# Optimization experiments

Hardware: AMD Instinct MI355X
Metric: run time of the kernel (lower is better)

Reference implementation:

```python
import jax, jax.numpy as jnp
import numpy as np
from jax.scipy.special import logsumexp

NODES = 128
K = 8
N = 4096  # num data samples; must equal M (original code stacks (N,) with (M,))
Z = NODES * (NODES - 1) // 2


def setup_inputs() -> dict:
    key = jax.random.key(0)
    k1, k2, k3 = jax.random.split(key, 3)
    X = jax.random.normal(k1, (N, NODES), dtype=jnp.float32)
    noise = jax.random.normal(k2, (N, NODES), dtype=jnp.float32)
    theta = jax.random.normal(k3, (K, 2, Z), dtype=jnp.float32)
    logc = jnp.zeros((K,), dtype=jnp.float32)
    return {"X": X, "noise": noise, "theta": theta, "logc": logc}


def reference(X, noise, theta, logc):
    n = X.shape[0]
    m = noise.shape[0]
    nodes = X.shape[1]
    iu, ju = np.triu_indices(nodes, k=1)  # static pair indices, z = nodes*(nodes-1)//2

    def mixture_logprob(A):
        # A: (S, nodes) -> per-component log prob summed over all node pairs, then
        # logsumexp over the K mixture components with weights logc.
        d = A[:, iu] - A[:, ju]                      # (S, z) pairwise phase diffs
        lp = (jnp.einsum('kz,sz->ks', theta[:, 0], jnp.cos(d))
              + jnp.einsum('kz,sz->ks', theta[:, 1], jnp.sin(d)))  # (K, S)
        return logsumexp(lp + logc[:, None], axis=0)  # (S,)

    lp_data = mixture_logprob(X)      # (n,)
    lp_noise = mixture_logprob(noise)  # (m,) == (n,)

    logN = jnp.log(jnp.float32(n))
    logM = jnp.log(jnp.float32(m))
    # log_nx = log_ny = 0 in the original code
    log_J1_denom = jnp.logaddexp(logN + lp_data, logM)
    log_J2_denom = jnp.logaddexp(logN + lp_noise, logM)
    J = (jnp.mean(logN + lp_data - log_J1_denom)
         + jnp.mean(logN - log_J2_denom))
    return J
```

## Files before the change

### kernel.cpp

```cpp
#include <hip/hip_runtime.h>
#include <hip/hip_bf16.h>
#include <math.h>

#define NODES 128
#define KMIX  8
#define NSAMP 4096
#define STOT  8192
#define ZPAIR 8128
#define FDIM  256

using bf16x8 = __attribute__((ext_vector_type(8))) short;
using f32x4  = __attribute__((ext_vector_type(4))) float;

#define OF_F   ((size_t)0)
#define OF_M   (OF_F + (size_t)STOT * FDIM / 2)
#define OF_LP4 (OF_M + (size_t)KMIX * FDIM * FDIM / 2)
#define OF_PT  (OF_LP4 + (size_t)4 * KMIX * STOT)
#define OF_CT  (OF_PT + 32)

__device__ __forceinline__ float bf2f(short u) {
    union { unsigned u32; float f; } cv;
    cv.u32 = ((unsigned)(unsigned short)u) << 16;
    return cv.f;
}
__device__ __forceinline__ short f2bf(float f) {
    union { float f; unsigned u32; } cv; cv.f = f;
    unsigned r = cv.u32 + 0x7fff + ((cv.u32 >> 16) & 1);
    return (short)(r >> 16);
}
__device__ __forceinline__ float softplusf(float x) {
    return fmaxf(x, 0.0f) + log1pf(expf(-fabsf(x)));
}

#define FEAT_BLOCKS (STOT * NODES / 256)
#define WB_BLOCKS   (KMIX * FDIM * FDIM / 256)

__global__ void prep_kernel(const float* __restrict__ X, const float* __restrict__ noise,
                            const float* __restrict__ theta,
                            short* __restrict__ F, short* __restrict__ W,
                            unsigned* __restrict__ ctr) {
    const int b = blockIdx.x, t = threadIdx.x;
    if (b == 0 && t == 0) *ctr = 0u;
    if (b < FEAT_BLOCKS) {
        int idx = b * 256 + t;
        int s = idx >> 7, i = idx & 127;
        float v = (s < NSAMP) ? X[idx] : noise[idx - NSAMP * NODES];
        float sv, cv;
        __sincosf(v, &sv, &cv);
        F[(size_t)s * FDIM + i]       = f2bf(cv);
        F[(size_t)s * FDIM + 128 + i] = f2bf(sv);
    } else {
        int idx = (b - FEAT_BLOCKS) * 256 + t;
        int j = idx & 255, i = (idx >> 8) & 255, k = idx >> 16;
        int a = i & 127, bb = j & 127;
        int hi = i >> 7, hj = j >> 7;
        float val = 0.0f;
        if (a != bb) {
            int p = a < bb ? a : bb;
            int q = a < bb ? bb : a;
            int z = p * 127 - (p * (p - 1)) / 2 + (q - p - 1);
            if (hi == hj) {
                val = 0.5f * theta[(size_t)(k * 2 + 0) * ZPAIR + z];
            } else if (hi == 1 && hj == 0) {
                float t1 = theta[(size_t)(k * 2 + 1) * ZPAIR + z];
                val = (a < bb) ? t1 : -t1;
            }
        }
        W[idx] = f2bf(val);
    }
}

__global__ __launch_bounds__(256, 2) void gemm_fused(
        const short* __restrict__ F, const short* __restrict__ M,
        float* __restrict__ lp2) {
    __shared__ short Ft[2][128 * 64];
    __shared__ short Mt[2][128 * 64];

    const int bid = blockIdx.x;
    const int k   = bid >> 6;
    const int st  = bid & 63;
    const int sbase = st * 128;

    const int t = threadIdx.x;
    const int wid = t >> 6, lane = t & 63;
    const int wm = wid >> 1, wn = wid & 1;

    const short* Mk = M + (size_t)k * FDIM * FDIM;

    const int rg = lane >> 3;
    const int sc = (lane & 7) ^ rg;

    f32x4 acc0[4][4] = {};
    f32x4 acc1[4][4] = {};

    auto stageF = [&](int buf, int c) {
        #pragma unroll
        for (int q = 0; q < 4; q++) {
            int g = wid * 4 + q;
            const short* src = F + ((size_t)(sbase + g * 8 + rg)) * FDIM + c * 64 + sc * 8;
            __builtin_amdgcn_global_load_lds((const unsigned*)src,
                                             (unsigned*)&Ft[buf][g * 512], 16, 0, 0);
        }
    };
    auto stageW = [&](int buf, int ihrow, int c) {
        #pragma unroll
        for (int q = 0; q < 4; q++) {
            int g = wid * 4 + q;
            const short* src = Mk + ((size_t)(ihrow * 128 + g * 8 + rg)) * FDIM + c * 64 + sc * 8;
            __builtin_amdgcn_global_load_lds((const unsigned*)src,
                                             (unsigned*)&Mt[buf][g * 512], 16, 0, 0);
        }
    };

    const int rlow = lane & 15, kq = lane >> 4;

    auto compute = [&](int fbuf, int mbuf, f32x4 (&acc)[4][4]) {
        bf16x8 afr[4][2], bfr[4][2];
        #pragma unroll
        for (int m = 0; m < 4; m++) {
            int row = wm * 64 + m * 16 + rlow;
            #pragma unroll
            for (int kk = 0; kk < 2; kk++) {
                int c16 = (kk * 4 + kq) ^ (row & 7);
                afr[m][kk] = *(const bf16x8*)&Ft[fbuf][row * 64 + c16 * 8];
            }
        }
        #pragma unroll
        for (int n = 0; n < 4; n++) {
            int row = wn * 64 + n * 16 + rlow;
            #pragma unroll
            for (int kk = 0; kk < 2; kk++) {
                int c16 = (kk * 4 + kq) ^ (row & 7);
                bfr[n][kk] = *(const bf16x8*)&Mt[mbuf][row * 64 + c16 * 8];
            }
        }
        #pragma unroll
        for (int m = 0; m < 4; m++)
            #pragma unroll
            for (int n = 0; n < 4; n++)
                #pragma unroll
                for (int kk = 0; kk < 2; kk++)
                    acc[m][n] = __builtin_amdgcn_mfma_f32_16x16x32_bf16(
                        afr[m][kk], bfr[n][kk], acc[m][n], 0, 0, 0);
    };

    stageF(0, 0); stageW(0, 0, 0);
    stageW(1, 1, 0);
    __syncthreads();
    compute(0, 0, acc0);
    __syncthreads();
    stageF(1, 1); stageW(0, 0, 1);
    __syncthreads();
    compute(0, 1, acc1);
    __syncthreads();
    stageW(1, 1, 1);
    __syncthreads();
    compute(1, 0, acc0);
    __syncthreads();
    stageF(0, 2); stageW(0, 1, 2);
    __syncthreads();
    compute(1, 1, acc1);
    __syncthreads();
    stageF(1, 3); stageW(1, 1, 3);
    __syncthreads();
    compute(0, 0, acc1);
    __syncthreads();
    compute(1, 1, acc1);

    float psum[4][4];
    #pragma unroll
    for (int m = 0; m < 4; m++) {
        #pragma unroll
        for (int q = 0; q < 4; q++) {
            int srow = wm * 64 + m * 16 + kq * 4 + q;
            const short* fr0 = F + (size_t)(sbase + srow) * FDIM + wn * 64 + rlow;
            float p = 0.0f;
            #pragma unroll
            for (int n = 0; n < 4; n++)
                p += bf2f(fr0[n * 16]) * acc0[m][n][q];
            #pragma unroll
            for (int n = 0; n < 4; n++)
                p += bf2f(fr0[128 + n * 16]) * acc1[m][n][q];
            psum[m][q] = p;
        }
    }
    #pragma unroll
    for (int off = 1; off < 16; off <<= 1)
        #pragma unroll
        for (int m = 0; m < 4; m++)
            #pragma unroll
            for (int q = 0; q < 4; q++)
                psum[m][q] += __shfl_xor(psum[m][q], off, 64);

    if (rlow == 0) {
        #pragma unroll
        for (int m = 0; m < 4; m++)
            #pragma unroll
            for (int q = 0; q < 4; q++) {
                int srow = wm * 64 + m * 16 + kq * 4 + q;
                lp2[((size_t)wn * KMIX + k) * STOT + sbase + srow] = psum[m][q];
            }
    }
}

__global__ void reduce_kernel(const float* __restrict__ lp2,
                              const float* __restrict__ logc,
                              float* __restrict__ partials,
                              unsigned* __restrict__ counter,
                              float* __restrict__ out) {
    const int t = threadIdx.x;
    const int s = blockIdx.x * 256 + t;

    float v[KMIX];
    #pragma unroll
    for (int k = 0; k < KMIX; k++) {
        v[k] = lp2[((size_t)0 * KMIX + k) * STOT + s]
             + lp2[((size_t)1 * KMIX + k) * STOT + s]
             + logc[k];
    }
    float mx = v[0];
    #pragma unroll
    for (int k = 1; k < KMIX; k++) mx = fmaxf(mx, v[k]);
    float sum = 0.0f;
    #pragma unroll
    for (int k = 0; k < KMIX; k++) sum += expf(v[k] - mx);
    const float lp = mx + logf(sum);

    const float term = (s < NSAMP) ? -softplusf(-lp) : -softplusf(lp);

    float bsum = term;
    #pragma unroll
    for (int off = 32; off; off >>= 1) bsum += __shfl_down(bsum, off);
    __shared__ float wsum[4];
    if ((t & 63) == 0) wsum[t >> 6] = bsum;
    __syncthreads();

    if (t == 0) {
        partials[blockIdx.x] = wsum[0] + wsum[1] + wsum[2] + wsum[3];
        __threadfence();
        unsigned old = atomicAdd(counter, 1u);
        if (old == 31u) {
            __threadfence();
            float tot = 0.0f;
            #pragma unroll
            for (int b = 0; b < 32; b++) tot += partials[b];
            out[0] = tot * (1.0f / (float)NSAMP);
        }
    }
}

extern "C" void kernel_launch(void* const* d_in, const int* in_sizes, int n_in,
                              void* d_out, int out_size, void* d_ws, size_t ws_size,
                              hipStream_t stream) {
    (void)in_sizes; (void)n_in; (void)out_size; (void)ws_size;
    const float* X     = (const float*)d_in[0];
    const float* noise = (const float*)d_in[1];
    const float* theta = (const float*)d_in[2];
    const float* logc  = (const float*)d_in[3];
    float* out = (float*)d_out;
    float* ws  = (float*)d_ws;

    short*    Fb    = (short*)(ws + OF_F);
    short*    Wb    = (short*)(ws + OF_M);
    float*    lp2   = ws + OF_LP4;
    float*    parts = ws + OF_PT;
    unsigned* ctr   = (unsigned*)(ws + OF_CT);

    prep_kernel<<<FEAT_BLOCKS + WB_BLOCKS, 256, 0, stream>>>(X, noise, theta, Fb, Wb, ctr);
    gemm_fused<<<KMIX * (STOT / 128), 256, 0, stream>>>(Fb, Wb, lp2);
    reduce_kernel<<<STOT / 256, 256, 0, stream>>>(lp2, logc, parts, ctr, out);
}
```

Measured before the change: 26.71 us.

## Overlap global-to-LDS staging with MFMA using explicit waitcnt and barriers

Splits the compute step into LDS fragment loads and MFMA issue. It replaces __syncthreads with hand-placed s_waitcnt vmcnt/lgkmcnt plus s_barrier, so the next tile's global_load_lds staging is issued before the current tile's MFMAs and overlaps them. This removes full drains of outstanding memory ops at each barrier. The risk is that the vmcnt counts are hand-tuned, and a miscount could read LDS data that is stale or not yet loaded.

```diff
diff --git a/kernel.cpp b/kernel.cpp
--- a/kernel.cpp
+++ b/kernel.cpp
@@ -17,6 +17,10 @@
 #define OF_LP4 (OF_M + (size_t)KMIX * FDIM * FDIM / 2)
 #define OF_PT  (OF_LP4 + (size_t)4 * KMIX * STOT)
 #define OF_CT  (OF_PT + 32)
+
+#define VMC(N) asm volatile("s_waitcnt vmcnt(" #N ")" ::: "memory")
+#define LGKM0  asm volatile("s_waitcnt lgkmcnt(0)" ::: "memory")
+#define SBAR   asm volatile("s_barrier" ::: "memory")
 
 __device__ __forceinline__ float bf2f(short u) {
     union { unsigned u32; float f; } cv;
@@ -114,8 +118,8 @@
 
     const int rlow = lane & 15, kq = lane >> 4;
 
-    auto compute = [&](int fbuf, int mbuf, f32x4 (&acc)[4][4]) {
-        bf16x8 afr[4][2], bfr[4][2];
+    bf16x8 afr[4][2], bfr[4][2];
+    auto loadA = [&](int fbuf) {
         #pragma unroll
         for (int m = 0; m < 4; m++) {
             int row = wm * 64 + m * 16 + rlow;
@@ -125,6 +129,8 @@
                 afr[m][kk] = *(const bf16x8*)&Ft[fbuf][row * 64 + c16 * 8];
             }
         }
+    };
+    auto loadB = [&](int mbuf) {
         #pragma unroll
         for (int n = 0; n < 4; n++) {
             int row = wn * 64 + n * 16 + rlow;
@@ -134,6 +140,8 @@
                 bfr[n][kk] = *(const bf16x8*)&Mt[mbuf][row * 64 + c16 * 8];
             }
         }
+    };
+    auto mfma = [&](f32x4 (&acc)[4][4]) {
         #pragma unroll
         for (int m = 0; m < 4; m++)
             #pragma unroll
@@ -144,28 +152,34 @@
                         afr[m][kk], bfr[n][kk], acc[m][n], 0, 0, 0);
     };
 
-    stageF(0, 0); stageW(0, 0, 0);
-    stageW(1, 1, 0);
-    __syncthreads();
-    compute(0, 0, acc0);
-    __syncthreads();
+    stageF(0, 0); stageW(0, 0, 0); stageW(1, 1, 0);
+
+    VMC(4); SBAR;
+    loadA(0); loadB(0);
+    LGKM0; SBAR;
     stageF(1, 1); stageW(0, 0, 1);
-    __syncthreads();
-    compute(0, 1, acc1);
-    __syncthreads();
+    mfma(acc0);
+    VMC(8); SBAR;
+    loadA(0); loadB(1);
+    LGKM0; SBAR;
     stageW(1, 1, 1);
-    __syncthreads();
-    compute(1, 0, acc0);
-    __syncthreads();
+    mfma(acc1);
+    VMC(4); SBAR;
+    loadA(1); loadB(0);
+    LGKM0; SBAR;
     stageF(0, 2); stageW(0, 1, 2);
-    __syncthreads();
-    compute(1, 1, acc1);
-    __syncthreads();
+    mfma(acc0);
+    VMC(8); SBAR;
+    loadA(1); loadB(1);
+    LGKM0; SBAR;
     stageF(1, 3); stageW(1, 1, 3);
-    __syncthreads();
-    compute(0, 0, acc1);
-    __syncthreads();
-    compute(1, 1, acc1);
+    mfma(acc1);
+    VMC(8); SBAR;
+    loadA(0); loadB(0);
+    mfma(acc1);
+    VMC(0); SBAR;
+    loadA(1); loadB(1);
+    mfma(acc1);
 
     float psum[4][4];
     #pragma unroll
```

Measured after the change: 26.53 us. Within noise of the previous version (-0.7%).

## Split GEMM across 8 waves, vectorize prep, and make lp layout sample-major

Applied to the files above, without the earlier changes.

The GEMM block grows from 4 to 8 waves, each owning a 64x32 output tile instead of 64x64. This halves per-wave accumulators and staging work, aiming at more latency hiding and occupancy, and MFMA runs get raised priority via s_setprio. The feature prep now processes four values per thread with vector loads and stores. Partial log-probs are stored sample-major with four column partials per component, so the reduce kernel reads contiguous float4s. The cost is more partial sums to combine and more shuffle work per wave.

```diff
diff --git a/kernel.cpp b/kernel.cpp
--- a/kernel.cpp
+++ b/kernel.cpp
@@ -14,8 +14,8 @@
 
 #define OF_F   ((size_t)0)
 #define OF_M   (OF_F + (size_t)STOT * FDIM / 2)
-#define OF_LP4 (OF_M + (size_t)KMIX * FDIM * FDIM / 2)
-#define OF_PT  (OF_LP4 + (size_t)4 * KMIX * STOT)
+#define OF_LP  (OF_M + (size_t)KMIX * FDIM * FDIM / 2)
+#define OF_PT  (OF_LP + (size_t)32 * STOT)
 #define OF_CT  (OF_PT + 32)
 
 __device__ __forceinline__ float bf2f(short u) {
@@ -32,8 +32,8 @@
     return fmaxf(x, 0.0f) + log1pf(expf(-fabsf(x)));
 }
 
-#define FEAT_BLOCKS (STOT * NODES / 256)
-#define WB_BLOCKS   (KMIX * FDIM * FDIM / 256)
+#define FEAT_BLOCKS4 (STOT * NODES / 4 / 256)
+#define WB_BLOCKS    (KMIX * FDIM * FDIM / 256)
 
 __global__ void prep_kernel(const float* __restrict__ X, const float* __restrict__ noise,
                             const float* __restrict__ theta,
@@ -41,16 +41,22 @@
                             unsigned* __restrict__ ctr) {
     const int b = blockIdx.x, t = threadIdx.x;
     if (b == 0 && t == 0) *ctr = 0u;
-    if (b < FEAT_BLOCKS) {
-        int idx = b * 256 + t;
-        int s = idx >> 7, i = idx & 127;
-        float v = (s < NSAMP) ? X[idx] : noise[idx - NSAMP * NODES];
-        float sv, cv;
-        __sincosf(v, &sv, &cv);
-        F[(size_t)s * FDIM + i]       = f2bf(cv);
-        F[(size_t)s * FDIM + 128 + i] = f2bf(sv);
+    if (b < FEAT_BLOCKS4) {
+        int idx4 = (b * 256 + t) * 4;
+        int s = idx4 >> 7, i = idx4 & 127;
+        const float* src = (s < NSAMP) ? (X + idx4) : (noise + (idx4 - NSAMP * NODES));
+        f32x4 v = *(const f32x4*)src;
+        short cb[4], sb[4];
+        #pragma unroll
+        for (int q = 0; q < 4; q++) {
+            float sv, cv;
+            __sincosf(v[q], &sv, &cv);
+            cb[q] = f2bf(cv); sb[q] = f2bf(sv);
+        }
+        *(short4*)&F[(size_t)s * FDIM + i]       = *(short4*)cb;
+        *(short4*)&F[(size_t)s * FDIM + 128 + i] = *(short4*)sb;
     } else {
-        int idx = (b - FEAT_BLOCKS) * 256 + t;
+        int idx = (b - FEAT_BLOCKS4) * 256 + t;
         int j = idx & 255, i = (idx >> 8) & 255, k = idx >> 16;
         int a = i & 127, bb = j & 127;
         int hi = i >> 7, hj = j >> 7;
@@ -70,9 +76,9 @@
     }
 }
 
-__global__ __launch_bounds__(256, 2) void gemm_fused(
+__global__ __launch_bounds__(512, 4) void gemm_fused(
         const short* __restrict__ F, const short* __restrict__ M,
-        float* __restrict__ lp2) {
+        float* __restrict__ lp32) {
     __shared__ short Ft[2][128 * 64];
     __shared__ short Mt[2][128 * 64];
 
@@ -83,20 +89,20 @@
 
     const int t = threadIdx.x;
     const int wid = t >> 6, lane = t & 63;
-    const int wm = wid >> 1, wn = wid & 1;
+    const int wm = wid >> 2, wn = wid & 3;
 
     const short* Mk = M + (size_t)k * FDIM * FDIM;
 
     const int rg = lane >> 3;
     const int sc = (lane & 7) ^ rg;
 
-    f32x4 acc0[4][4] = {};
-    f32x4 acc1[4][4] = {};
+    f32x4 acc0[4][2] = {};
+    f32x4 acc1[4][2] = {};
 
     auto stageF = [&](int buf, int c) {
         #pragma unroll
-        for (int q = 0; q < 4; q++) {
-            int g = wid * 4 + q;
+        for (int q = 0; q < 2; q++) {
+            int g = wid * 2 + q;
             const short* src = F + ((size_t)(sbase + g * 8 + rg)) * FDIM + c * 64 + sc * 8;
             __builtin_amdgcn_global_load_lds((const unsigned*)src,
                                              (unsigned*)&Ft[buf][g * 512], 16, 0, 0);
@@ -104,8 +110,8 @@
     };
     auto stageW = [&](int buf, int ihrow, int c) {
         #pragma unroll
-        for (int q = 0; q < 4; q++) {
-            int g = wid * 4 + q;
+        for (int q = 0; q < 2; q++) {
+            int g = wid * 2 + q;
             const short* src = Mk + ((size_t)(ihrow * 128 + g * 8 + rg)) * FDIM + c * 64 + sc * 8;
             __builtin_amdgcn_global_load_lds((const unsigned*)src,
                                              (unsigned*)&Mt[buf][g * 512], 16, 0, 0);
@@ -114,8 +120,8 @@
 
     const int rlow = lane & 15, kq = lane >> 4;
 
-    auto compute = [&](int fbuf, int mbuf, f32x4 (&acc)[4][4]) {
-        bf16x8 afr[4][2], bfr[4][2];
+    bf16x8 afr[4][2], bfr[2][2];
+    auto loadA = [&](int fbuf) {
         #pragma unroll
         for (int m = 0; m < 4; m++) {
             int row = wm * 64 + m * 16 + rlow;
@@ -125,23 +131,32 @@
                 afr[m][kk] = *(const bf16x8*)&Ft[fbuf][row * 64 + c16 * 8];
             }
         }
-        #pragma unroll
-        for (int n = 0; n < 4; n++) {
-            int row = wn * 64 + n * 16 + rlow;
+    };
+    auto loadB = [&](int mbuf) {
+        #pragma unroll
+        for (int n = 0; n < 2; n++) {
+            int row = wn * 32 + n * 16 + rlow;
             #pragma unroll
             for (int kk = 0; kk < 2; kk++) {
                 int c16 = (kk * 4 + kq) ^ (row & 7);
                 bfr[n][kk] = *(const bf16x8*)&Mt[mbuf][row * 64 + c16 * 8];
             }
         }
+    };
+    auto mfma = [&](f32x4 (&acc)[4][2]) {
+        __builtin_amdgcn_s_setprio(1);
         #pragma unroll
         for (int m = 0; m < 4; m++)
             #pragma unroll
-            for (int n = 0; n < 4; n++)
+            for (int n = 0; n < 2; n++)
                 #pragma unroll
                 for (int kk = 0; kk < 2; kk++)
                     acc[m][n] = __builtin_amdgcn_mfma_f32_16x16x32_bf16(
                         afr[m][kk], bfr[n][kk], acc[m][n], 0, 0, 0);
+        __builtin_amdgcn_s_setprio(0);
+    };
+    auto compute = [&](int fbuf, int mbuf, f32x4 (&acc)[4][2]) {
+        loadA(fbuf); loadB(mbuf); mfma(acc);
     };
 
     stageF(0, 0); stageW(0, 0, 0);
@@ -173,13 +188,13 @@
         #pragma unroll
         for (int q = 0; q < 4; q++) {
             int srow = wm * 64 + m * 16 + kq * 4 + q;
-            const short* fr0 = F + (size_t)(sbase + srow) * FDIM + wn * 64 + rlow;
+            const short* fr0 = F + (size_t)(sbase + srow) * FDIM + wn * 32 + rlow;
             float p = 0.0f;
             #pragma unroll
-            for (int n = 0; n < 4; n++)
+            for (int n = 0; n < 2; n++)
                 p += bf2f(fr0[n * 16]) * acc0[m][n][q];
             #pragma unroll
-            for (int n = 0; n < 4; n++)
+            for (int n = 0; n < 2; n++)
                 p += bf2f(fr0[128 + n * 16]) * acc1[m][n][q];
             psum[m][q] = p;
         }
@@ -198,12 +213,12 @@
             #pragma unroll
             for (int q = 0; q < 4; q++) {
                 int srow = wm * 64 + m * 16 + kq * 4 + q;
-                lp2[((size_t)wn * KMIX + k) * STOT + sbase + srow] = psum[m][q];
-            }
-    }
-}
-
-__global__ void reduce_kernel(const float* __restrict__ lp2,
+                lp32[(size_t)(sbase + srow) * 32 + k * 4 + wn] = psum[m][q];
+            }
+    }
+}
+
+__global__ void reduce_kernel(const float* __restrict__ lp32,
                               const float* __restrict__ logc,
                               float* __restrict__ partials,
                               unsigned* __restrict__ counter,
@@ -211,13 +226,14 @@
     const int t = threadIdx.x;
     const int s = blockIdx.x * 256 + t;
 
+    const f32x4* base = (const f32x4*)&lp32[(size_t)s * 32];
     float v[KMIX];
     #pragma unroll
     for (int k = 0; k < KMIX; k++) {
-        v[k] = lp2[((size_t)0 * KMIX + k) * STOT + s]
-             + lp2[((size_t)1 * KMIX + k) * STOT + s]
-             + logc[k];
-    }
+        f32x4 r = base[k];
+        v[k] = (r[0] + r[1]) + (r[2] + r[3]) + logc[k];
+    }
+
     float mx = v[0];
     #pragma unroll
     for (int k = 1; k < KMIX; k++) mx = fmaxf(mx, v[k]);
@@ -262,11 +278,11 @@
 
     short*    Fb    = (short*)(ws + OF_F);
     short*    Wb    = (short*)(ws + OF_M);
-    float*    lp2   = ws + OF_LP4;
+    float*    lp32  = ws + OF_LP;
     float*    parts = ws + OF_PT;
     unsigned* ctr   = (unsigned*)(ws + OF_CT);
 
-    prep_kernel<<<FEAT_BLOCKS + WB_BLOCKS, 256, 0, stream>>>(X, noise, theta, Fb, Wb, ctr);
-    gemm_fused<<<KMIX * (STOT / 128), 256, 0, stream>>>(Fb, Wb, lp2);
-    reduce_kernel<<<STOT / 256, 256, 0, stream>>>(lp2, logc, parts, ctr, out);
-}
+    prep_kernel<<<FEAT_BLOCKS4 + WB_BLOCKS, 256, 0, stream>>>(X, noise, theta, Fb, Wb, ctr);
+    gemm_fused<<<KMIX * (STOT / 128), 512, 0, stream>>>(Fb, Wb, lp32);
+    reduce_kernel<<<STOT / 256, 256, 0, stream>>>(lp32, logc, parts, ctr, out);
+}
```

Result: slower. 29.31 us (+9.7%).
